# Optimization experiments

Measured on AMD Instinct MI355X. Metric: run time of the kernel, lower is better.

## Reference

```python
import jax, jax.numpy as jnp
import numpy as np

B, N, D, NS, H, ITERS = 64, 4096, 64, 7, 128, 3
EPS = 1e-8
SCALE = D ** -0.5
LN_EPS = 1e-5


def layernorm(x, g, b):
    m = x.mean(-1, keepdims=True)
    v = ((x - m) ** 2).mean(-1, keepdims=True)
    return (x - m) / jnp.sqrt(v + LN_EPS) * g + b


def gru_cell(x, h, W_ih, W_hh, b_ih, b_hh):
    # torch.nn.GRUCell semantics
    gi = x @ W_ih.T + b_ih
    gh = h @ W_hh.T + b_hh
    i_r, i_z, i_n = jnp.split(gi, 3, axis=-1)
    h_r, h_z, h_n = jnp.split(gh, 3, axis=-1)
    r = jax.nn.sigmoid(i_r + h_r)
    z = jax.nn.sigmoid(i_z + h_z)
    n = jnp.tanh(i_n + r * h_n)
    return (1.0 - z) * n + z * h


def setup_inputs() -> dict:
    key = jax.random.key(0)
    ks = jax.random.split(key, 16)
    s = 0.02
    inp = {}
    inp['inputs'] = jax.random.normal(ks[0], (B, N, D), jnp.float32)
    inp['positional_embeddings'] = jax.random.normal(ks[1], (B, N, 4), jnp.float32)
    inp['slots_noise'] = jax.random.normal(ks[2], (B, NS, D), jnp.float32)
    inp['slots_mu'] = jax.random.normal(ks[3], (1, 1, D), jnp.float32)
    inp['slots_sigma'] = jax.random.uniform(ks[4], (1, 1, D), jnp.float32)
    inp['Wq'] = jax.random.normal(ks[5], (D, D), jnp.float32) * s
    inp['bq'] = jnp.zeros((D,), jnp.float32)
    inp['Wk'] = jax.random.normal(ks[6], (D, D), jnp.float32) * s
    inp['bk'] = jnp.zeros((D,), jnp.float32)
    inp['Wv'] = jax.random.normal(ks[7], (D, D), jnp.float32) * s
    inp['bv'] = jnp.zeros((D,), jnp.float32)
    inp['W_ih'] = jax.random.normal(ks[8], (3 * D, D), jnp.float32) * s
    inp['W_hh'] = jax.random.normal(ks[9], (3 * D, D), jnp.float32) * s
    inp['b_ih'] = jnp.zeros((3 * D,), jnp.float32)
    inp['b_hh'] = jnp.zeros((3 * D,), jnp.float32)
    inp['W1'] = jax.random.normal(ks[10], (H, D), jnp.float32) * s
    inp['b1'] = jnp.zeros((H,), jnp.float32)
    inp['W2'] = jax.random.normal(ks[11], (D, H), jnp.float32) * s
    inp['b2'] = jnp.zeros((D,), jnp.float32)
    inp['g_in'] = jnp.ones((D,), jnp.float32)
    inp['be_in'] = jnp.zeros((D,), jnp.float32)
    inp['g_sl'] = jnp.ones((D,), jnp.float32)
    inp['be_sl'] = jnp.zeros((D,), jnp.float32)
    inp['g_ff'] = jnp.ones((D,), jnp.float32)
    inp['be_ff'] = jnp.zeros((D,), jnp.float32)
    return inp


def reference(inputs, positional_embeddings, slots_noise, slots_mu, slots_sigma,
              Wq, bq, Wk, bk, Wv, bv, W_ih, W_hh, b_ih, b_hh,
              W1, b1, W2, b2, g_in, be_in, g_sl, be_sl, g_ff, be_ff):
    b, n, d = inputs.shape
    # slots ~ Normal(mu, sigma), reparameterized with externalized noise
    slots = slots_mu + slots_sigma * slots_noise  # [b, NS, d]
    x = layernorm(inputs, g_in, be_in)
    k = x @ Wk.T + bk  # [b, n, d]
    v = x @ Wv.T + bv  # [b, n, d]
    for _ in range(ITERS):
        slots_prev = slots
        s = layernorm(slots, g_sl, be_sl)
        q = s @ Wq.T + bq  # [b, NS, d]
        dots = jnp.einsum('bid,bjd->bij', q, k) * SCALE  # [b, NS, n]
        attn = jax.nn.softmax(dots, axis=1) + EPS  # softmax over slot axis
        attn = attn / attn.sum(-1, keepdims=True)  # renormalize over inputs
        updates = jnp.einsum('bjd,bij->bid', v, attn)  # [b, NS, d]
        slots = gru_cell(updates.reshape(-1, d), slots_prev.reshape(-1, d),
                         W_ih, W_hh, b_ih, b_hh).reshape(b, -1, d)
        ff = layernorm(slots, g_ff, be_ff)
        slots = slots + (jax.nn.relu(ff @ W1.T + b1) @ W2.T + b2)
    return slots
```

## Files before the change

### kernel.cpp

```cpp
#include <hip/hip_runtime.h>
#include <stdint.h>

#define BB 64
#define NN 4096
#define DD 64
#define NSL 7
#define HH 128
#define NITER 3
#define TPT 2

typedef __attribute__((ext_vector_type(8))) short short8;
typedef __attribute__((ext_vector_type(4))) float f32x4;

__device__ __forceinline__ unsigned short f2bf(float f){
    union { float f; unsigned int i; } x; x.f = f;
    unsigned int u = x.i;
    u += 0x7fffu + ((u >> 16) & 1u);
    return (unsigned short)(u >> 16);
}
__device__ __forceinline__ unsigned int pack2(float a, float b){
    return (unsigned int)f2bf(a) | ((unsigned int)f2bf(b) << 16);
}
__device__ __forceinline__ short8 f2bf8(float4 a, float4 b){
    short8 r;
    r[0]=(short)f2bf(a.x); r[1]=(short)f2bf(a.y); r[2]=(short)f2bf(a.z); r[3]=(short)f2bf(a.w);
    r[4]=(short)f2bf(b.x); r[5]=(short)f2bf(b.y); r[6]=(short)f2bf(b.z); r[7]=(short)f2bf(b.w);
    return r;
}
__device__ __forceinline__ f32x4 mfma16(short8 a, short8 b, f32x4 c){
    return __builtin_amdgcn_mfma_f32_16x16x32_bf16(a, b, c, 0, 0, 0);
}
__device__ __forceinline__ float sigm(float x){ return 1.f / (1.f + __expf(-x)); }

__global__ __launch_bounds__(256) void ln_kv_kernel(
    const float* __restrict__ inp,
    const float* __restrict__ g_in, const float* __restrict__ be_in,
    const float* __restrict__ Wk, const float* __restrict__ bk,
    const float* __restrict__ Wv, const float* __restrict__ bv,
    unsigned short* __restrict__ k_out, unsigned short* __restrict__ vT_out)
{
    const int t = threadIdx.x, lane = t & 63, wave = t >> 6;
    const int n16 = lane & 15, quad = lane >> 4;
    const long T0 = (long)blockIdx.x * (TPT*64);

    float4 X[TPT][4];
    #pragma unroll
    for (int c = 0; c < TPT; ++c){
        const float* rp = inp + (T0 + c*64 + wave*16 + n16) * 64;
        X[c][0] = *reinterpret_cast<const float4*>(rp + quad*8);
        X[c][1] = *reinterpret_cast<const float4*>(rp + quad*8 + 4);
        X[c][2] = *reinterpret_cast<const float4*>(rp + 32 + quad*8);
        X[c][3] = *reinterpret_cast<const float4*>(rp + 32 + quad*8 + 4);
    }

    const float4 gA = *reinterpret_cast<const float4*>(g_in + quad*8);
    const float4 gB = *reinterpret_cast<const float4*>(g_in + quad*8 + 4);
    const float4 gC = *reinterpret_cast<const float4*>(g_in + 32 + quad*8);
    const float4 gD = *reinterpret_cast<const float4*>(g_in + 32 + quad*8 + 4);
    const float4 eA = *reinterpret_cast<const float4*>(be_in + quad*8);
    const float4 eB = *reinterpret_cast<const float4*>(be_in + quad*8 + 4);
    const float4 eC = *reinterpret_cast<const float4*>(be_in + 32 + quad*8);
    const float4 eD = *reinterpret_cast<const float4*>(be_in + 32 + quad*8 + 4);

    short8 wka0[4], wka1[4], wvb0[4], wvb1[4];
    float4 bk4[4];
    float  bvs[4];
    #pragma unroll
    for (int mt = 0; mt < 4; ++mt){
        const float* wp = Wk + (mt*16 + n16)*64 + quad*8;
        wka0[mt] = f2bf8(*reinterpret_cast<const float4*>(wp),
                         *reinterpret_cast<const float4*>(wp + 4));
        wka1[mt] = f2bf8(*reinterpret_cast<const float4*>(wp + 32),
                         *reinterpret_cast<const float4*>(wp + 36));
        const float* vp = Wv + (mt*16 + n16)*64 + quad*8;
        wvb0[mt] = f2bf8(*reinterpret_cast<const float4*>(vp),
                         *reinterpret_cast<const float4*>(vp + 4));
        wvb1[mt] = f2bf8(*reinterpret_cast<const float4*>(vp + 32),
                         *reinterpret_cast<const float4*>(vp + 36));
        bk4[mt] = *reinterpret_cast<const float4*>(bk + mt*16 + quad*4);
        bvs[mt] = bv[mt*16 + n16];
    }

    #pragma unroll
    for (int c = 0; c < TPT; ++c){
        const long Tc = T0 + c*64;
        float4 xa = X[c][0], xb = X[c][1], xc = X[c][2], xd = X[c][3];

        float s  = (xa.x+xa.y+xa.z+xa.w) + (xb.x+xb.y+xb.z+xb.w)
                 + (xc.x+xc.y+xc.z+xc.w) + (xd.x+xd.y+xd.z+xd.w);
        float ss = (xa.x*xa.x+xa.y*xa.y+xa.z*xa.z+xa.w*xa.w)
                 + (xb.x*xb.x+xb.y*xb.y+xb.z*xb.z+xb.w*xb.w)
                 + (xc.x*xc.x+xc.y*xc.y+xc.z*xc.z+xc.w*xc.w)
                 + (xd.x*xd.x+xd.y*xd.y+xd.z*xd.z+xd.w*xd.w);
        s  += __shfl_xor(s, 16);  ss += __shfl_xor(ss, 16);
        s  += __shfl_xor(s, 32);  ss += __shfl_xor(ss, 32);
        const float mean = s * 0.015625f;
        const float rstd = rsqrtf(ss * 0.015625f - mean*mean + 1e-5f);

        float4 ya, yb, yc, yd;
        ya.x=(xa.x-mean)*rstd*gA.x+eA.x; ya.y=(xa.y-mean)*rstd*gA.y+eA.y;
        ya.z=(xa.z-mean)*rstd*gA.z+eA.z; ya.w=(xa.w-mean)*rstd*gA.w+eA.w;
        yb.x=(xb.x-mean)*rstd*gB.x+eB.x; yb.y=(xb.y-mean)*rstd*gB.y+eB.y;
        yb.z=(xb.z-mean)*rstd*gB.z+eB.z; yb.w=(xb.w-mean)*rstd*gB.w+eB.w;
        yc.x=(xc.x-mean)*rstd*gC.x+eC.x; yc.y=(xc.y-mean)*rstd*gC.y+eC.y;
        yc.z=(xc.z-mean)*rstd*gC.z+eC.z; yc.w=(xc.w-mean)*rstd*gC.w+eC.w;
        yd.x=(xd.x-mean)*rstd*gD.x+eD.x; yd.y=(xd.y-mean)*rstd*gD.y+eD.y;
        yd.z=(xd.z-mean)*rstd*gD.z+eD.z; yd.w=(xd.w-mean)*rstd*gD.w+eD.w;
        const short8 xf0 = f2bf8(ya, yb);
        const short8 xf1 = f2bf8(yc, yd);

        unsigned short* krow = k_out + (Tc + wave*16 + n16)*64;
        #pragma unroll
        for (int mt = 0; mt < 4; ++mt){
            f32x4 z = {0.f,0.f,0.f,0.f};
            z = mfma16(wka0[mt], xf0, z);
            z = mfma16(wka1[mt], xf1, z);
            uint2 pk;
            pk.x = pack2(z[0]+bk4[mt].x, z[1]+bk4[mt].y);
            pk.y = pack2(z[2]+bk4[mt].z, z[3]+bk4[mt].w);
            *reinterpret_cast<uint2*>(krow + mt*16 + quad*4) = pk;
        }
        const int bidx = (int)(Tc >> 12);
        const int jblk = ((int)Tc & 4095) + wave*16 + quad*4;
        #pragma unroll
        for (int dt = 0; dt < 4; ++dt){
            f32x4 z = {0.f,0.f,0.f,0.f};
            z = mfma16(xf0, wvb0[dt], z);
            z = mfma16(xf1, wvb1[dt], z);
            uint2 pk;
            pk.x = pack2(z[0]+bvs[dt], z[1]+bvs[dt]);
            pk.y = pack2(z[2]+bvs[dt], z[3]+bvs[dt]);
            *reinterpret_cast<uint2*>(vT_out + ((long)(bidx*64 + dt*16 + n16))*4096 + jblk) = pk;
        }
    }
}

__global__ __launch_bounds__(256) void scan_kernel(
    const unsigned short* __restrict__ k_ws, const unsigned short* __restrict__ vT_ws,
    const float* __restrict__ q_ws, float* __restrict__ pu)
{
    __shared__ __align__(16) unsigned short at_all[4][16 * 40];
    __shared__ float red[4][8][80];
    const int t = threadIdx.x, lane = t & 63, wave = t >> 6;
    const int n16 = lane & 15, quad = lane >> 4;
    const int b = blockIdx.x >> 5, seg = blockIdx.x & 31;
    unsigned short* at = at_all[wave];

    const int j0 = seg*128 + wave*32;
    const long kbase = (long)b * NN * 64;
    const long vbase = (long)b * 64 * NN;

    const int iq = (n16 < NSL) ? n16 : (NSL - 1);
    const float* qp = q_ws + (b*NSL + iq)*64;
    float4 q0 = *reinterpret_cast<const float4*>(qp + quad*8);
    float4 q1 = *reinterpret_cast<const float4*>(qp + quad*8 + 4);
    float4 q2 = *reinterpret_cast<const float4*>(qp + 32 + quad*8);
    float4 q3 = *reinterpret_cast<const float4*>(qp + 32 + quad*8 + 4);

    short8 kb0[2], kb1[2];
    #pragma unroll
    for (int tt = 0; tt < 2; ++tt){
        const unsigned short* kp = k_ws + kbase + (long)(j0 + tt*16 + n16)*64 + quad*8;
        kb0[tt] = *reinterpret_cast<const short8*>(kp);
        kb1[tt] = *reinterpret_cast<const short8*>(kp + 32);
    }
    short8 vb[4];
    #pragma unroll
    for (int t2 = 0; t2 < 4; ++t2)
        vb[t2] = *reinterpret_cast<const short8*>(
            vT_ws + vbase + (long)(t2*16 + n16)*NN + j0 + quad*8);

    for (int idx = lane; idx < 9 * 40; idx += 64){
        int rr = idx / 40, cc = idx - rr * 40;
        at[(7 + rr) * 40 + cc] = (rr == 0 && cc < 32) ? (unsigned short)0x3F80 : (unsigned short)0;
    }

    short8 qa0 = f2bf8(make_float4(q0.x*0.125f,q0.y*0.125f,q0.z*0.125f,q0.w*0.125f),
                       make_float4(q1.x*0.125f,q1.y*0.125f,q1.z*0.125f,q1.w*0.125f));
    short8 qa1 = f2bf8(make_float4(q2.x*0.125f,q2.y*0.125f,q2.z*0.125f,q2.w*0.125f),
                       make_float4(q3.x*0.125f,q3.y*0.125f,q3.z*0.125f,q3.w*0.125f));

    #pragma unroll
    for (int tt = 0; tt < 2; ++tt){
        f32x4 dz = {0.f,0.f,0.f,0.f};
        dz = mfma16(qa0, kb0[tt], dz);
        dz = mfma16(qa1, kb1[tt], dz);
        float pm;
        if (quad == 0)      pm = fmaxf(fmaxf(dz[0], dz[1]), fmaxf(dz[2], dz[3]));
        else if (quad == 1) pm = fmaxf(fmaxf(dz[0], dz[1]), dz[2]);
        else                pm = -1e30f;
        pm = fmaxf(pm, __shfl_xor(pm, 16));
        float e0=0.f, e1=0.f, e2=0.f, e3=0.f;
        if (quad == 0){ e0=__expf(dz[0]-pm); e1=__expf(dz[1]-pm); e2=__expf(dz[2]-pm); e3=__expf(dz[3]-pm); }
        else if (quad == 1){ e0=__expf(dz[0]-pm); e1=__expf(dz[1]-pm); e2=__expf(dz[2]-pm); }
        float ps = e0 + e1 + e2 + e3;
        ps += __shfl_xor(ps, 16);
        const float inv = 1.f / ps;
        if (quad == 0){
            at[0*40 + tt*16 + n16] = f2bf(e0*inv);
            at[1*40 + tt*16 + n16] = f2bf(e1*inv);
            at[2*40 + tt*16 + n16] = f2bf(e2*inv);
            at[3*40 + tt*16 + n16] = f2bf(e3*inv);
        } else if (quad == 1){
            at[4*40 + tt*16 + n16] = f2bf(e0*inv);
            at[5*40 + tt*16 + n16] = f2bf(e1*inv);
            at[6*40 + tt*16 + n16] = f2bf(e2*inv);
        }
    }

    short8 aa = *reinterpret_cast<const short8*>(at + n16*40 + quad*8);
    short8 ones;
    { const short ov = (n16 == 0) ? (short)0x3F80 : (short)0;
      #pragma unroll
      for (int z = 0; z < 8; ++z) ones[z] = ov; }

    f32x4 uacc[5];
    #pragma unroll
    for (int t2 = 0; t2 < 4; ++t2){
        f32x4 z = {0.f,0.f,0.f,0.f};
        uacc[t2] = mfma16(aa, vb[t2], z);
    }
    { f32x4 z = {0.f,0.f,0.f,0.f}; uacc[4] = mfma16(aa, ones, z); }

    if (quad < 2){
        #pragma unroll
        for (int r = 0; r < 4; ++r){
            const int i = quad*4 + r;
            #pragma unroll
            for (int t2 = 0; t2 < 5; ++t2)
                red[wave][i][t2*16 + n16] = uacc[t2][r];
        }
    }
    __syncthreads();
    for (int idx = t; idx < 640; idx += 256){
        const int i = idx / 80, cc = idx - i*80;
        float s = red[0][i][cc] + red[1][i][cc] + red[2][i][cc] + red[3][i][cc];
        pu[((long)(b*32 + seg)*8 + i)*80 + cc] = s;
    }
}

__device__ __forceinline__ float dot64(const float* x, const float* w){
    float acc = 0.f;
    const float4* w4 = reinterpret_cast<const float4*>(w);
    #pragma unroll
    for (int e4 = 0; e4 < 16; ++e4){
        float4 wv = w4[e4];
        acc += x[e4*4+0]*wv.x + x[e4*4+1]*wv.y + x[e4*4+2]*wv.z + x[e4*4+3]*wv.w;
    }
    return acc;
}
__device__ __forceinline__ float dot128(const float* x, const float* w){
    float acc = 0.f;
    const float4* w4 = reinterpret_cast<const float4*>(w);
    #pragma unroll
    for (int e4 = 0; e4 < 32; ++e4){
        float4 wv = w4[e4];
        acc += x[e4*4+0]*wv.x + x[e4*4+1]*wv.y + x[e4*4+2]*wv.z + x[e4*4+3]*wv.w;
    }
    return acc;
}

__global__ __launch_bounds__(256) void slot_update_kernel(
    const int mode, const int write_out,
    const float* __restrict__ pu,
    float* __restrict__ slots_ws, float* __restrict__ q_ws,
    const float* __restrict__ noise, const float* __restrict__ mu,
    const float* __restrict__ sigma,
    const float* __restrict__ W_ih, const float* __restrict__ W_hh,
    const float* __restrict__ b_ih, const float* __restrict__ b_hh,
    const float* __restrict__ W1, const float* __restrict__ b1,
    const float* __restrict__ W2, const float* __restrict__ b2,
    const float* __restrict__ g_sl, const float* __restrict__ be_sl,
    const float* __restrict__ g_ff, const float* __restrict__ be_ff,
    const float* __restrict__ Wq, const float* __restrict__ bq,
    float* __restrict__ out)
{
    __shared__ float hprev[64], updv[64], snew[64], ffb[64], h1[128], sfin[64], s2[64];
    __shared__ float redp[4][64], redp7[4][64];
    __shared__ float gi[192], gh[192];
    __shared__ float redA_s;
    const int t = threadIdx.x;
    const int b = blockIdx.x / NSL, i = blockIdx.x % NSL;
    const int lane = t & 63, wave = t >> 6;
    const long rowoff = (long)(b*NSL + i)*64;

    if (mode == 0){
        if (t < 64){
            float v = mu[t] + sigma[t] * noise[rowoff + t];
            sfin[t] = v;
            slots_ws[rowoff + t] = v;
        }
    } else {
        if (t < 64) hprev[t] = slots_ws[rowoff + t];
        {
            const int d = t & 63, g = t >> 6;
            float si = 0.f, s7 = 0.f;
            #pragma unroll
            for (int u = 0; u < 8; ++u){
                const float* base = pu + ((long)(b*32 + g*8 + u)*8)*80;
                si += base[i*80 + d];
                s7 += base[7*80 + d];
            }
            redp[g][d] = si; redp7[g][d] = s7;
        }
        if (wave == 0){
            float a = (lane < 32) ? pu[((long)(b*32 + lane)*8 + i)*80 + 64] : 0.f;
            #pragma unroll
            for (int m = 1; m < 64; m <<= 1) a += __shfl_xor(a, m);
            if (lane == 0) redA_s = a;
        }
        __syncthreads();
        if (t < 64){
            float ri = redp[0][t] + redp[1][t] + redp[2][t] + redp[3][t];
            float r7 = redp7[0][t] + redp7[1][t] + redp7[2][t] + redp7[3][t];
            updv[t] = (ri + 1e-8f * r7) / (redA_s + 4.096e-5f);
        }
        __syncthreads();
        for (int c = t; c < 384; c += 256){
            if (c < 192) gi[c] = b_ih[c] + dot64(updv, W_ih + c*64);
            else { int cc = c - 192; gh[cc] = b_hh[cc] + dot64(hprev, W_hh + cc*64); }
        }
        __syncthreads();
        if (t < 64){
            float rg = sigm(gi[t] + gh[t]);
            float zg = sigm(gi[64+t] + gh[64+t]);
            float ng = tanhf(gi[128+t] + rg * gh[128+t]);
            snew[t] = (1.f - zg) * ng + zg * hprev[t];
        }
        __syncthreads();
        {
            float x = snew[lane];
            float s = x, ss = x * x;
            #pragma unroll
            for (int m = 1; m < 64; m <<= 1){ s += __shfl_xor(s, m); ss += __shfl_xor(ss, m); }
            float mean = s * 0.015625f;
            float var  = ss * 0.015625f - mean * mean;
            float rstd = rsqrtf(var + 1e-5f);
            if (wave == 0) ffb[lane] = (x - mean) * rstd * g_ff[lane] + be_ff[lane];
        }
        __syncthreads();
        if (t < 128){
            float vv = b1[t] + dot64(ffb, W1 + t*64);
            h1[t] = vv > 0.f ? vv : 0.f;
        }
        __syncthreads();
        if (t < 64){
            float o = b2[t] + dot128(h1, W2 + t*128);
            float v = snew[t] + o;
            sfin[t] = v;
            slots_ws[rowoff + t] = v;
            if (write_out) out[rowoff + t] = v;
        }
    }
    __syncthreads();
    {
        float x = sfin[lane];
        float s = x, ss = x * x;
        #pragma unroll
        for (int m = 1; m < 64; m <<= 1){ s += __shfl_xor(s, m); ss += __shfl_xor(ss, m); }
        float mean = s * 0.015625f;
        float var  = ss * 0.015625f - mean * mean;
        float rstd = rsqrtf(var + 1e-5f);
        if (wave == 0) s2[lane] = (x - mean) * rstd * g_sl[lane] + be_sl[lane];
    }
    __syncthreads();
    if (t < 64) q_ws[rowoff + t] = bq[t] + dot64(s2, Wq + t*64);
}

extern "C" void kernel_launch(void* const* d_in, const int* in_sizes, int n_in,
                              void* d_out, int out_size, void* d_ws, size_t ws_size,
                              hipStream_t stream)
{
    const float* inp   = (const float*)d_in[0];
    const float* noise = (const float*)d_in[2];
    const float* mu    = (const float*)d_in[3];
    const float* sigma = (const float*)d_in[4];
    const float* Wq    = (const float*)d_in[5];
    const float* bq    = (const float*)d_in[6];
    const float* Wk    = (const float*)d_in[7];
    const float* bk    = (const float*)d_in[8];
    const float* Wv    = (const float*)d_in[9];
    const float* bv    = (const float*)d_in[10];
    const float* W_ih  = (const float*)d_in[11];
    const float* W_hh  = (const float*)d_in[12];
    const float* b_ih  = (const float*)d_in[13];
    const float* b_hh  = (const float*)d_in[14];
    const float* W1    = (const float*)d_in[15];
    const float* b1    = (const float*)d_in[16];
    const float* W2    = (const float*)d_in[17];
    const float* b2    = (const float*)d_in[18];
    const float* g_in  = (const float*)d_in[19];
    const float* be_in = (const float*)d_in[20];
    const float* g_sl  = (const float*)d_in[21];
    const float* be_sl = (const float*)d_in[22];
    const float* g_ff  = (const float*)d_in[23];
    const float* be_ff = (const float*)d_in[24];
    float* out = (float*)d_out;

    char* w = (char*)d_ws;
    unsigned short* k_ws  = (unsigned short*)(w);
    unsigned short* vT_ws = (unsigned short*)(w + 33554432);
    float* slots_ws       = (float*)(w + 67108864);
    float* q_ws           = (float*)(w + 67108864 + 114688);
    float* pu             = (float*)(w + 67108864 + 229376);

    ln_kv_kernel<<<4096/TPT, 256, 0, stream>>>(inp, g_in, be_in, Wk, bk, Wv, bv, k_ws, vT_ws);
    slot_update_kernel<<<448, 256, 0, stream>>>(0, 0, pu, slots_ws, q_ws, noise, mu, sigma,
        W_ih, W_hh, b_ih, b_hh, W1, b1, W2, b2, g_sl, be_sl, g_ff, be_ff, Wq, bq, out);
    for (int it = 0; it < NITER; ++it){
        scan_kernel<<<2048, 256, 0, stream>>>(k_ws, vT_ws, q_ws, pu);
        slot_update_kernel<<<448, 256, 0, stream>>>(1, (it == NITER - 1) ? 1 : 0,
            pu, slots_ws, q_ws, noise, mu, sigma,
            W_ih, W_hh, b_ih, b_hh, W1, b1, W2, b2, g_sl, be_sl, g_ff, be_ff, Wq, bq, out);
    }
}
```

Baseline: 272.1 us.

## Enlarge per-block work in LN/KV and scan kernels with software-prefetched input

```diff
diff --git a/kernel.cpp b/kernel.cpp
--- a/kernel.cpp
+++ b/kernel.cpp
@@ -7,7 +7,8 @@
 #define NSL 7
 #define HH 128
 #define NITER 3
-#define TPT 2
+#define TPT 4
+#define NSEG 16
 
 typedef __attribute__((ext_vector_type(8))) short short8;
 typedef __attribute__((ext_vector_type(4))) float f32x4;
@@ -43,14 +44,13 @@
     const int n16 = lane & 15, quad = lane >> 4;
     const long T0 = (long)blockIdx.x * (TPT*64);
 
-    float4 X[TPT][4];
-    #pragma unroll
-    for (int c = 0; c < TPT; ++c){
-        const float* rp = inp + (T0 + c*64 + wave*16 + n16) * 64;
-        X[c][0] = *reinterpret_cast<const float4*>(rp + quad*8);
-        X[c][1] = *reinterpret_cast<const float4*>(rp + quad*8 + 4);
-        X[c][2] = *reinterpret_cast<const float4*>(rp + 32 + quad*8);
-        X[c][3] = *reinterpret_cast<const float4*>(rp + 32 + quad*8 + 4);
+    float4 Xc0, Xc1, Xc2, Xc3;
+    {
+        const float* rp = inp + (T0 + wave*16 + n16) * 64;
+        Xc0 = *reinterpret_cast<const float4*>(rp + quad*8);
+        Xc1 = *reinterpret_cast<const float4*>(rp + quad*8 + 4);
+        Xc2 = *reinterpret_cast<const float4*>(rp + 32 + quad*8);
+        Xc3 = *reinterpret_cast<const float4*>(rp + 32 + quad*8 + 4);
     }
 
     const float4 gA = *reinterpret_cast<const float4*>(g_in + quad*8);
@@ -83,8 +83,16 @@
 
     #pragma unroll
     for (int c = 0; c < TPT; ++c){
+        float4 Xn0, Xn1, Xn2, Xn3;
+        if (c + 1 < TPT){
+            const float* rp = inp + (T0 + (c+1)*64 + wave*16 + n16) * 64;
+            Xn0 = *reinterpret_cast<const float4*>(rp + quad*8);
+            Xn1 = *reinterpret_cast<const float4*>(rp + quad*8 + 4);
+            Xn2 = *reinterpret_cast<const float4*>(rp + 32 + quad*8);
+            Xn3 = *reinterpret_cast<const float4*>(rp + 32 + quad*8 + 4);
+        }
         const long Tc = T0 + c*64;
-        float4 xa = X[c][0], xb = X[c][1], xc = X[c][2], xd = X[c][3];
+        float4 xa = Xc0, xb = Xc1, xc = Xc2, xd = Xc3;
 
         float s  = (xa.x+xa.y+xa.z+xa.w) + (xb.x+xb.y+xb.z+xb.w)
                  + (xc.x+xc.y+xc.z+xc.w) + (xd.x+xd.y+xd.z+xd.w);
@@ -132,6 +140,7 @@
             pk.y = pack2(z[2]+bvs[dt], z[3]+bvs[dt]);
             *reinterpret_cast<uint2*>(vT_out + ((long)(bidx*64 + dt*16 + n16))*4096 + jblk) = pk;
         }
+        Xc0 = Xn0; Xc1 = Xn1; Xc2 = Xn2; Xc3 = Xn3;
     }
 }
 
@@ -139,14 +148,14 @@
     const unsigned short* __restrict__ k_ws, const unsigned short* __restrict__ vT_ws,
     const float* __restrict__ q_ws, float* __restrict__ pu)
 {
-    __shared__ __align__(16) unsigned short at_all[4][16 * 40];
+    __shared__ __align__(16) unsigned short at_all[4][16 * 72];
     __shared__ float red[4][8][80];
     const int t = threadIdx.x, lane = t & 63, wave = t >> 6;
     const int n16 = lane & 15, quad = lane >> 4;
-    const int b = blockIdx.x >> 5, seg = blockIdx.x & 31;
+    const int b = blockIdx.x >> 4, seg = blockIdx.x & 15;
     unsigned short* at = at_all[wave];
 
-    const int j0 = seg*128 + wave*32;
+    const int j0 = seg*256 + wave*64;
     const long kbase = (long)b * NN * 64;
     const long vbase = (long)b * 64 * NN;
 
@@ -157,22 +166,24 @@
     float4 q2 = *reinterpret_cast<const float4*>(qp + 32 + quad*8);
     float4 q3 = *reinterpret_cast<const float4*>(qp + 32 + quad*8 + 4);
 
-    short8 kb0[2], kb1[2];
-    #pragma unroll
-    for (int tt = 0; tt < 2; ++tt){
+    short8 kb0[4], kb1[4];
+    #pragma unroll
+    for (int tt = 0; tt < 4; ++tt){
         const unsigned short* kp = k_ws + kbase + (long)(j0 + tt*16 + n16)*64 + quad*8;
         kb0[tt] = *reinterpret_cast<const short8*>(kp);
         kb1[tt] = *reinterpret_cast<const short8*>(kp + 32);
     }
-    short8 vb[4];
-    #pragma unroll
-    for (int t2 = 0; t2 < 4; ++t2)
-        vb[t2] = *reinterpret_cast<const short8*>(
-            vT_ws + vbase + (long)(t2*16 + n16)*NN + j0 + quad*8);
-
-    for (int idx = lane; idx < 9 * 40; idx += 64){
-        int rr = idx / 40, cc = idx - rr * 40;
-        at[(7 + rr) * 40 + cc] = (rr == 0 && cc < 32) ? (unsigned short)0x3F80 : (unsigned short)0;
+    short8 vba[4], vbb[4];
+    #pragma unroll
+    for (int t2 = 0; t2 < 4; ++t2){
+        const unsigned short* vp = vT_ws + vbase + (long)(t2*16 + n16)*NN + j0 + quad*8;
+        vba[t2] = *reinterpret_cast<const short8*>(vp);
+        vbb[t2] = *reinterpret_cast<const short8*>(vp + 32);
+    }
+
+    for (int idx = lane; idx < 9 * 72; idx += 64){
+        int rr = idx / 72, cc = idx - rr * 72;
+        at[(7 + rr) * 72 + cc] = (rr == 0 && cc < 64) ? (unsigned short)0x3F80 : (unsigned short)0;
     }
 
     short8 qa0 = f2bf8(make_float4(q0.x*0.125f,q0.y*0.125f,q0.z*0.125f,q0.w*0.125f),
@@ -181,7 +192,7 @@
                        make_float4(q3.x*0.125f,q3.y*0.125f,q3.z*0.125f,q3.w*0.125f));
 
     #pragma unroll
-    for (int tt = 0; tt < 2; ++tt){
+    for (int tt = 0; tt < 4; ++tt){
         f32x4 dz = {0.f,0.f,0.f,0.f};
         dz = mfma16(qa0, kb0[tt], dz);
         dz = mfma16(qa1, kb1[tt], dz);
@@ -197,18 +208,19 @@
         ps += __shfl_xor(ps, 16);
         const float inv = 1.f / ps;
         if (quad == 0){
-            at[0*40 + tt*16 + n16] = f2bf(e0*inv);
-            at[1*40 + tt*16 + n16] = f2bf(e1*inv);
-            at[2*40 + tt*16 + n16] = f2bf(e2*inv);
-            at[3*40 + tt*16 + n16] = f2bf(e3*inv);
+            at[0*72 + tt*16 + n16] = f2bf(e0*inv);
+            at[1*72 + tt*16 + n16] = f2bf(e1*inv);
+            at[2*72 + tt*16 + n16] = f2bf(e2*inv);
+            at[3*72 + tt*16 + n16] = f2bf(e3*inv);
         } else if (quad == 1){
-            at[4*40 + tt*16 + n16] = f2bf(e0*inv);
-            at[5*40 + tt*16 + n16] = f2bf(e1*inv);
-            at[6*40 + tt*16 + n16] = f2bf(e2*inv);
-        }
-    }
-
-    short8 aa = *reinterpret_cast<const short8*>(at + n16*40 + quad*8);
+            at[4*72 + tt*16 + n16] = f2bf(e0*inv);
+            at[5*72 + tt*16 + n16] = f2bf(e1*inv);
+            at[6*72 + tt*16 + n16] = f2bf(e2*inv);
+        }
+    }
+
+    short8 aa0 = *reinterpret_cast<const short8*>(at + n16*72 + quad*8);
+    short8 aa1 = *reinterpret_cast<const short8*>(at + n16*72 + 32 + quad*8);
     short8 ones;
     { const short ov = (n16 == 0) ? (short)0x3F80 : (short)0;
       #pragma unroll
@@ -218,9 +230,14 @@
     #pragma unroll
     for (int t2 = 0; t2 < 4; ++t2){
         f32x4 z = {0.f,0.f,0.f,0.f};
-        uacc[t2] = mfma16(aa, vb[t2], z);
-    }
-    { f32x4 z = {0.f,0.f,0.f,0.f}; uacc[4] = mfma16(aa, ones, z); }
+        z = mfma16(aa0, vba[t2], z);
+        uacc[t2] = mfma16(aa1, vbb[t2], z);
+    }
+    {
+        f32x4 z = {0.f,0.f,0.f,0.f};
+        z = mfma16(aa0, ones, z);
+        uacc[4] = mfma16(aa1, ones, z);
+    }
 
     if (quad < 2){
         #pragma unroll
@@ -235,7 +252,7 @@
     for (int idx = t; idx < 640; idx += 256){
         const int i = idx / 80, cc = idx - i*80;
         float s = red[0][i][cc] + red[1][i][cc] + red[2][i][cc] + red[3][i][cc];
-        pu[((long)(b*32 + seg)*8 + i)*80 + cc] = s;
+        pu[((long)(b*NSEG + seg)*8 + i)*80 + cc] = s;
     }
 }
 
@@ -296,15 +313,15 @@
             const int d = t & 63, g = t >> 6;
             float si = 0.f, s7 = 0.f;
             #pragma unroll
-            for (int u = 0; u < 8; ++u){
-                const float* base = pu + ((long)(b*32 + g*8 + u)*8)*80;
+            for (int u = 0; u < 4; ++u){
+                const float* base = pu + ((long)(b*NSEG + g*4 + u)*8)*80;
                 si += base[i*80 + d];
                 s7 += base[7*80 + d];
             }
             redp[g][d] = si; redp7[g][d] = s7;
         }
         if (wave == 0){
-            float a = (lane < 32) ? pu[((long)(b*32 + lane)*8 + i)*80 + 64] : 0.f;
+            float a = (lane < NSEG) ? pu[((long)(b*NSEG + lane)*8 + i)*80 + 64] : 0.f;
             #pragma unroll
             for (int m = 1; m < 64; m <<= 1) a += __shfl_xor(a, m);
             if (lane == 0) redA_s = a;
@@ -408,7 +425,7 @@
     slot_update_kernel<<<448, 256, 0, stream>>>(0, 0, pu, slots_ws, q_ws, noise, mu, sigma,
         W_ih, W_hh, b_ih, b_hh, W1, b1, W2, b2, g_sl, be_sl, g_ff, be_ff, Wq, bq, out);
     for (int it = 0; it < NITER; ++it){
-        scan_kernel<<<2048, 256, 0, stream>>>(k_ws, vT_ws, q_ws, pu);
+        scan_kernel<<<64*NSEG, 256, 0, stream>>>(k_ws, vT_ws, q_ws, pu);
         slot_update_kernel<<<448, 256, 0, stream>>>(1, (it == NITER - 1) ? 1 : 0,
             pu, slots_ws, q_ws, noise, mu, sigma,
             W_ih, W_hh, b_ih, b_hh, W1, b1, W2, b2, g_sl, be_sl, g_ff, be_ff, Wq, bq, out);
```

New measurement: 259.9 us. 1.05x faster.
